# Kernel optimization log

Hardware: AMD Instinct MI355X
Metric: run time of the kernel (lower is better)

The kernel has to match this reference:

```python
import jax, jax.numpy as jnp
import numpy as np

N = 50000      # nodes
E = 500000     # edges
H = 128        # hidden_channels
P = 1024       # number of (src,dst) link pairs: z==1 and z==2 counts
L = 3          # num_layers
MAXZ = 1000


def setup_inputs() -> dict:
    key = jax.random.key(0)
    ks = jax.random.split(key, 16)
    # z: P src nodes (label 1), P dst nodes (label 2), rest random labels >= 3
    z = jnp.concatenate([
        jnp.ones((P,), jnp.int32),
        jnp.full((P,), 2, jnp.int32),
        jax.random.randint(ks[0], (N - 2 * P,), 3, MAXZ, dtype=jnp.int32),
    ])
    edge_index = jax.random.randint(ks[1], (2, E), 0, N, dtype=jnp.int32)
    batch = jnp.zeros((N,), jnp.int32)  # unused in executed branch
    s = 1.0 / np.sqrt(H)
    z_table = jax.random.normal(ks[2], (MAXZ, H), jnp.float32) * 0.1
    conv_Wl = jax.random.normal(ks[3], (L, H, H), jnp.float32) * s
    conv_bl = jax.random.normal(ks[4], (L, H), jnp.float32) * 0.01
    conv_Wr = jax.random.normal(ks[5], (L, H, H), jnp.float32) * s
    W0 = jax.random.normal(ks[6], (H, H), jnp.float32) * s
    b0 = jax.random.normal(ks[7], (H,), jnp.float32) * 0.01
    W1 = jax.random.normal(ks[8], (H, H), jnp.float32) * s
    b1 = jax.random.normal(ks[9], (H,), jnp.float32) * 0.01
    W2 = jax.random.normal(ks[10], (1, H), jnp.float32) * s
    b2 = jax.random.normal(ks[11], (1,), jnp.float32) * 0.01
    return dict(z=z, edge_index=edge_index, batch=batch, z_table=z_table,
                conv_Wl=conv_Wl, conv_bl=conv_bl, conv_Wr=conv_Wr,
                W0=W0, b0=b0, W1=W1, b1=b1, W2=W2, b2=b2)


def _sage_conv(x, Wl, bl, Wr, src, dst):
    # x: [2, N, H]; mean-aggregate neighbor messages then linear (PyG SAGEConv)
    msgs = x[:, src, :]  # [2, E, H] gather
    agg = jax.vmap(lambda m: jax.ops.segment_sum(m, dst, num_segments=N))(msgs)
    deg = jax.ops.segment_sum(jnp.ones((dst.shape[0],), x.dtype), dst, num_segments=N)
    agg = agg / jnp.maximum(deg, 1.0)[None, :, None]
    return agg @ Wl.T + bl + x @ Wr.T  # lin_l(mean) + bias + lin_r(x)


def reference(z, edge_index, batch, z_table, conv_Wl, conv_bl, conv_Wr,
              W0, b0, W1, b1, W2, b2):
    src, dst = edge_index[0], edge_index[1]
    # ([[1],[2]] == z).long() -> [2, N] in {0,1}; embed -> [2, N, H]
    lbl = (jnp.arange(1, 3, dtype=z.dtype)[:, None] == z[None, :]).astype(jnp.int32)
    x = z_table[lbl]
    for i in range(L - 1):
        x = jax.nn.relu(_sage_conv(x, conv_Wl[i], conv_bl[i], conv_Wr[i], src, dst))
    x = _sage_conv(x, conv_Wl[L - 1], conv_bl[L - 1], conv_Wr[L - 1], src, dst)
    h = jax.nn.relu(x @ W0.T + b0).sum(axis=0)  # [N, H]
    src_idx = jnp.nonzero(z == 1, size=P)[0]
    dst_idx = jnp.nonzero(z == 2, size=P)[0]
    p = h[src_idx] * h[dst_idx]                 # [P, H]
    return jax.nn.relu(p @ W1.T + b1) @ W2.T + b2  # [P, 1]
```

## Files before the change

kernel.cpp:

```cpp
#include <hip/hip_runtime.h>
#include <stdint.h>

#define HH 128
typedef unsigned long long ull;
typedef unsigned short u16;

__device__ __forceinline__ ull shfl_up64(ull v, int d) {
  unsigned lo = (unsigned)__shfl_up((int)(unsigned)(v & 0xffffffffULL), d);
  unsigned hi = (unsigned)__shfl_up((int)(unsigned)(v >> 32), d);
  return ((ull)hi << 32) | (ull)lo;
}
__device__ __forceinline__ ull shfl_down64(ull v, int d) {
  unsigned lo = (unsigned)__shfl_down((int)(unsigned)(v & 0xffffffffULL), d);
  unsigned hi = (unsigned)__shfl_down((int)(unsigned)(v >> 32), d);
  return ((ull)hi << 32) | (ull)lo;
}

__global__ __launch_bounds__(256) void k_ytab(
    const float* __restrict__ zt, const float* __restrict__ Wl0,
    const float* __restrict__ Wr0, const float* __restrict__ Wl2,
    const float* __restrict__ Wr2, const float* __restrict__ bl0,
    const float* __restrict__ bl1, float* __restrict__ y_l,
    float* __restrict__ y_rb, float* __restrict__ vecs_g,
    const int* __restrict__ z, int N, ull* __restrict__ cnt64,
    int* __restrict__ mark, int* __restrict__ status, int* __restrict__ bctr) {
  __shared__ float ztS[2][HH];
  __shared__ float vS[4][HH];
  __shared__ float xS[16][HH];
  __shared__ float wAS[32][HH + 1], wBS[32][HH + 1];
  int t = threadIdx.x;
  {
    int gid = blockIdx.x * 256 + t;
    int nthr = gridDim.x * 256;
    for (int n = gid; n < N; n += nthr) {
      cnt64[n] = 0ULL;
      mark[n] = (z[n] <= 2) ? 1 : 0;
    }
    if (gid < 64) status[gid] = 0;
    if (gid == 0) *bctr = 0;
  }
  ztS[t >> 7][t & 127] = zt[t];
  __syncthreads();
  int j = t & 127, half = t >> 7;
  int jw = t >> 3, kk0 = (t & 7) * 4;
  float accA = 0.f, accR = 0.f;
  for (int kt = 0; kt < 4; kt++) {
    __syncthreads();
#pragma unroll
    for (int q = 0; q < 4; q++) {
      int jj = q * 32 + jw;
      float4 va = *(const float4*)(Wl0 + (size_t)jj * HH + kt * 32 + kk0);
      float4 vb = *(const float4*)(Wr0 + (size_t)jj * HH + kt * 32 + kk0);
      wAS[kk0 + 0][jj] = va.x; wAS[kk0 + 1][jj] = va.y;
      wAS[kk0 + 2][jj] = va.z; wAS[kk0 + 3][jj] = va.w;
      wBS[kk0 + 0][jj] = vb.x; wBS[kk0 + 1][jj] = vb.y;
      wBS[kk0 + 2][jj] = vb.z; wBS[kk0 + 3][jj] = vb.w;
    }
    __syncthreads();
#pragma unroll
    for (int kk = 0; kk < 32; kk++) {
      float zk = ztS[half][kt * 32 + kk];
      accA = fmaf(zk, wAS[kk][j], accA);
      accR = fmaf(zk, wBS[kk][j], accR);
    }
  }
  __syncthreads();
  vS[half][j] = accA;
  vS[2 + half][j] = accR;
  __syncthreads();
  if (blockIdx.x == 0) {
    vecs_g[t] = vS[t >> 7][t & 127];
    vecs_g[256 + t] = vS[2 + (t >> 7)][t & 127];
  }
  int v0 = blockIdx.x * 16;
#pragma unroll
  for (int rep = 0; rep < 8; rep++) {
    int idx = t + rep * 256;
    int r = idx >> 7, jx = idx & 127;
    int v = v0 + r;
    int d = v >> 4, cnt = (v >> 1) & 7, sel = v & 1;
    float invd = 1.0f / (float)max(d, 1);
    float u1 = (float)cnt * invd, u0 = (float)(d - cnt) * invd;
    xS[r][jx] = fmaxf(fmaf(u0, vS[0][jx], fmaf(u1, vS[1][jx], bl0[jx] + vS[2 + sel][jx])), 0.f);
  }
  int rh = t >> 7;
  float al[8], ar[8];
#pragma unroll
  for (int q = 0; q < 8; q++) { al[q] = 0.f; ar[q] = 0.f; }
  for (int kt = 0; kt < 4; kt++) {
    __syncthreads();
#pragma unroll
    for (int q = 0; q < 4; q++) {
      int jj = q * 32 + jw;
      float4 va = *(const float4*)(Wl2 + (size_t)jj * HH + kt * 32 + kk0);
      float4 vb = *(const float4*)(Wr2 + (size_t)jj * HH + kt * 32 + kk0);
      wAS[kk0 + 0][jj] = va.x; wAS[kk0 + 1][jj] = va.y;
      wAS[kk0 + 2][jj] = va.z; wAS[kk0 + 3][jj] = va.w;
      wBS[kk0 + 0][jj] = vb.x; wBS[kk0 + 1][jj] = vb.y;
      wBS[kk0 + 2][jj] = vb.z; wBS[kk0 + 3][jj] = vb.w;
    }
    __syncthreads();
#pragma unroll
    for (int kk = 0; kk < 32; kk++) {
      float wl = wAS[kk][j], wr = wBS[kk][j];
#pragma unroll
      for (int q = 0; q < 8; q++) {
        float x = xS[rh * 8 + q][kt * 32 + kk];
        al[q] = fmaf(x, wl, al[q]);
        ar[q] = fmaf(x, wr, ar[q]);
      }
    }
  }
  float bb = bl1[j];
#pragma unroll
  for (int q = 0; q < 8; q++) {
    int v = v0 + rh * 8 + q;
    y_l[((size_t)v << 7) + j] = al[q];
    y_rb[((size_t)v << 7) + j] = ar[q] + bb;
  }
}

__global__ void k_edge(const int* __restrict__ z, const int* __restrict__ src,
                       const int* __restrict__ dst, int E,
                       ull* __restrict__ cnt64, int* __restrict__ mark,
                       int* __restrict__ pos) {
  int e = blockIdx.x * blockDim.x + threadIdx.x;
  if (e >= E) return;
  int s = src[e], d = dst[e];
  int zs = z[s];
  ull val = 1ULL | ((ull)(zs == 1) << 20) | ((ull)(zs == 2) << 40);
  ull old = atomicAdd(&cnt64[d], val);
  pos[e] = (int)(old & 0xFFFFF);
  if (z[d] <= 2) mark[s] = 1;
}

__global__ __launch_bounds__(256) void k_scanpost(
    const ull* __restrict__ cnt64, const int* __restrict__ mark,
    const int* __restrict__ z, int N, int P,
    int* __restrict__ rowptr, int* __restrict__ mlist, int* __restrict__ minv,
    int* __restrict__ plist, int* __restrict__ Rm, int4* __restrict__ pack,
    u16* __restrict__ keyN, int* __restrict__ bctr,
    ull* __restrict__ aggbuf, int* __restrict__ status) {
  __shared__ ull wsum[4];
  __shared__ int chunk_s;
  __shared__ ull excl_s;
  int t = threadIdx.x;
  if (t == 0) chunk_s = atomicAdd(bctr, 1);
  __syncthreads();
  int b = chunk_s;
  int base = b * 1024 + t * 4;
  ull l[4]; ull s = 0;
#pragma unroll
  for (int i = 0; i < 4; i++) {
    int idx = base + i; ull v = 0;
    if (idx < N) {
      int zz = z[idx];
      v = (cnt64[idx] & 0xFFFFFULL) | ((ull)mark[idx] << 20)
        | ((ull)(zz == 1) << 40) | ((ull)(zz == 2) << 52);
    }
    l[i] = s; s += v;
  }
  int lane = t & 63, wid = t >> 6;
  ull vi = s;
  for (int d2 = 1; d2 < 64; d2 <<= 1) { ull o = shfl_up64(vi, d2); if (lane >= d2) vi += o; }
  if (lane == 63) wsum[wid] = vi;
  __syncthreads();
  ull woff = 0;
  for (int w = 0; w < wid; w++) woff += wsum[w];
  ull thrbase = woff + vi - s;
  if (t == 0) {
    ull btot = wsum[0] + wsum[1] + wsum[2] + wsum[3];
    __hip_atomic_store(&aggbuf[b], btot, __ATOMIC_RELAXED, __HIP_MEMORY_SCOPE_AGENT);
    __hip_atomic_store(&status[b], 1, __ATOMIC_RELEASE, __HIP_MEMORY_SCOPE_AGENT);
  }
  if (t < 64) {
    ull excl = 0;
    for (int p = lane; p < b; p += 64) {
      while (__hip_atomic_load(&status[p], __ATOMIC_ACQUIRE, __HIP_MEMORY_SCOPE_AGENT) == 0)
        __builtin_amdgcn_s_sleep(1);
      excl += __hip_atomic_load(&aggbuf[p], __ATOMIC_RELAXED, __HIP_MEMORY_SCOPE_AGENT);
    }
    for (int o = 32; o > 0; o >>= 1) excl += shfl_down64(excl, o);
    if (lane == 0) excl_s = excl;
  }
  __syncthreads();
  ull blockbase = excl_s;
#pragma unroll
  for (int i = 0; i < 4; i++) {
    int idx = base + i;
    if (idx >= N) break;
    ull sf = blockbase + thrbase + l[i];
    int rp = (int)(sf & 0xFFFFF);
    int mp = (int)((sf >> 20) & 0xFFFFF);
    int r1 = (int)((sf >> 40) & 0xFFF);
    int r2 = (int)(sf >> 52);
    rowptr[idx] = rp;
    int mk = mark[idx];
    if (mk) { mlist[mp] = idx; minv[idx] = mp; }
    int zz = z[idx];
    if (zz == 1) plist[r1] = idx;
    else if (zz == 2) plist[P + r2] = idx;
    ull cv = cnt64[idx];
    int dd = (int)(cv & 0xFFFFF), c1 = (int)((cv >> 20) & 0xFFFFF), c2 = (int)((cv >> 40) & 0xFFFFF);
    pack[idx] = make_int4(dd, c1, c2, zz);
    int wcls = (zz == 1) ? 1 : ((zz == 2) ? 2 : 0);
    u16 key;
    if (dd < 64 && c1 < 8 && c2 < 8) key = (u16)(dd | (c1 << 6) | (c2 << 9) | (wcls << 12));
    else key = 0x8000;
    keyN[idx] = key;
    if (idx == N - 1) *Rm = mp + mk;
  }
}

__global__ void k_csrk(const int* __restrict__ src, const int* __restrict__ dst, int E,
                       const int* __restrict__ rowptr, const int* __restrict__ pos,
                       const u16* __restrict__ keyN, const int* __restrict__ mark,
                       ull* __restrict__ csrk) {
  int e = blockIdx.x * blockDim.x + threadIdx.x;
  if (e >= E) return;
  int d = dst[e];
  if (!mark[d]) return;
  int s = src[e];
  csrk[rowptr[d] + pos[e]] = (ull)(unsigned)s | ((ull)keyN[s] << 32);
}

__device__ __noinline__ float4 yrow_fb(const float* __restrict__ vecs,
    const float* __restrict__ bl0, const float* __restrict__ Wm,
    int j4, int d, int cnt, int sel) {
  float invd = 1.0f / (float)max(d, 1);
  float u1 = (float)cnt * invd, u0 = (float)(d - cnt) * invd;
  const float* Rv = vecs + (2 + sel) * HH;
  float4 acc = make_float4(0, 0, 0, 0);
  for (int k = 0; k < HH; k++) {
    float x = fmaxf(fmaf(u0, vecs[k], fmaf(u1, vecs[HH + k], bl0[k] + Rv[k])), 0.f);
    acc.x = fmaf(x, Wm[(j4 + 0) * HH + k], acc.x);
    acc.y = fmaf(x, Wm[(j4 + 1) * HH + k], acc.y);
    acc.z = fmaf(x, Wm[(j4 + 2) * HH + k], acc.z);
    acc.w = fmaf(x, Wm[(j4 + 3) * HH + k], acc.w);
  }
  return acc;
}

__device__ __forceinline__ float4 yl_fetch(ull cv, int ch, int chsel, int j4,
    const float* __restrict__ y_l, const int4* __restrict__ pack,
    const float* __restrict__ vecs, const float* __restrict__ bl0,
    const float* __restrict__ Wl2) {
  int key = (int)(cv >> 32);
  if (key & 0x8000) {
    int s = (int)(cv & 0xFFFFFFFFULL);
    int4 p = pack[s];
    int cc = ch ? p.z : p.y;
    int sel = (p.w == chsel) ? 1 : 0;
    return yrow_fb(vecs, bl0, Wl2, j4, p.x, cc, sel);
  }
  int cc = (key >> (6 + 3 * ch)) & 7;
  int sel = (((key >> 12) & 3) == chsel) ? 1 : 0;
  int row = ((key & 63) << 4) + (cc << 1) + sel;
  return *(const float4*)(y_l + ((size_t)row << 7) + j4);
}

__global__ __launch_bounds__(256) void k_agg2Y(const int4* __restrict__ pack,
    const ull* __restrict__ csrk, const float* __restrict__ y_l,
    const float* __restrict__ y_rb, const float* __restrict__ vecs,
    const float* __restrict__ bl0, const float* __restrict__ bl1,
    const float* __restrict__ Wl2, const float* __restrict__ Wr2,
    const int* __restrict__ rowptr, const int* __restrict__ mlist,
    const int* __restrict__ Rdev, float* __restrict__ x2c) {
  int gt = blockIdx.x * blockDim.x + threadIdx.x;
  int w = gt >> 6, lane = gt & 63;
  int nw = (gridDim.x * blockDim.x) >> 6;
  int T = *Rdev;
  int ch = lane >> 5, j4 = (lane & 31) * 4;
  int chsel = ch + 1;
  for (int task = w; task < T; task += nw) {
    int n = mlist[task];
    int4 pn = pack[n];
    int beg = rowptr[n], d = pn.x;
    float4 acc = make_float4(0, 0, 0, 0);
    int i = 0;
    for (; i + 4 <= d; i += 4) {
      ull c0 = csrk[beg + i], c1 = csrk[beg + i + 1];
      ull c2 = csrk[beg + i + 2], c3 = csrk[beg + i + 3];
      float4 v0 = yl_fetch(c0, ch, chsel, j4, y_l, pack, vecs, bl0, Wl2);
      float4 v1 = yl_fetch(c1, ch, chsel, j4, y_l, pack, vecs, bl0, Wl2);
      float4 v2 = yl_fetch(c2, ch, chsel, j4, y_l, pack, vecs, bl0, Wl2);
      float4 v3 = yl_fetch(c3, ch, chsel, j4, y_l, pack, vecs, bl0, Wl2);
      acc.x += v0.x + v1.x + v2.x + v3.x;
      acc.y += v0.y + v1.y + v2.y + v3.y;
      acc.z += v0.z + v1.z + v2.z + v3.z;
      acc.w += v0.w + v1.w + v2.w + v3.w;
    }
    for (; i < d; i++) {
      float4 v0 = yl_fetch(csrk[beg + i], ch, chsel, j4, y_l, pack, vecs, bl0, Wl2);
      acc.x += v0.x; acc.y += v0.y; acc.z += v0.z; acc.w += v0.w;
    }
    float inv = 1.0f / (float)max(d, 1);
    int ccn = ch ? pn.z : pn.y;
    int seln = (pn.w == chsel) ? 1 : 0;
    float4 yr;
    if (pn.x < 64 && ccn < 8) {
      yr = *(const float4*)(y_rb + ((size_t)(((pn.x << 3) + ccn) * 2 + seln) << 7) + j4);
    } else {
      yr = yrow_fb(vecs, bl0, Wr2, j4, pn.x, ccn, seln);
      yr.x += bl1[j4]; yr.y += bl1[j4 + 1]; yr.z += bl1[j4 + 2]; yr.w += bl1[j4 + 3];
    }
    float4 o;
    o.x = fmaxf(fmaf(acc.x, inv, yr.x), 0.f);
    o.y = fmaxf(fmaf(acc.y, inv, yr.y), 0.f);
    o.z = fmaxf(fmaf(acc.z, inv, yr.z), 0.f);
    o.w = fmaxf(fmaf(acc.w, inv, yr.w), 0.f);
    *(float4*)(x2c + (size_t)task * 256 + ch * HH + j4) = o;
  }
}

__global__ __launch_bounds__(256) void k_agg3(const float* __restrict__ x2c,
    const ull* __restrict__ csrk, const int* __restrict__ rowptr,
    const int4* __restrict__ pack, const int* __restrict__ plist,
    const int* __restrict__ minv, int T, float* __restrict__ aggp) {
  int gt = blockIdx.x * blockDim.x + threadIdx.x;
  int w = gt >> 6, lane = gt & 63;
  int nw = (gridDim.x * blockDim.x) >> 6;
  int j4 = lane * 4;
  for (int task = w; task < T; task += nw) {
    int n = plist[task];
    int beg = rowptr[n], d = pack[n].x;
    float4 acc = make_float4(0, 0, 0, 0);
    int i = 0;
    for (; i + 4 <= d; i += 4) {
      int m0 = minv[(int)(csrk[beg + i] & 0xFFFFFFFFULL)];
      int m1 = minv[(int)(csrk[beg + i + 1] & 0xFFFFFFFFULL)];
      int m2 = minv[(int)(csrk[beg + i + 2] & 0xFFFFFFFFULL)];
      int m3 = minv[(int)(csrk[beg + i + 3] & 0xFFFFFFFFULL)];
      float4 v0 = *(const float4*)(x2c + (size_t)m0 * 256 + j4);
      float4 v1 = *(const float4*)(x2c + (size_t)m1 * 256 + j4);
      float4 v2 = *(const float4*)(x2c + (size_t)m2 * 256 + j4);
      float4 v3 = *(const float4*)(x2c + (size_t)m3 * 256 + j4);
      acc.x += v0.x + v1.x + v2.x + v3.x;
      acc.y += v0.y + v1.y + v2.y + v3.y;
      acc.z += v0.z + v1.z + v2.z + v3.z;
      acc.w += v0.w + v1.w + v2.w + v3.w;
    }
    for (; i < d; i++) {
      int m0 = minv[(int)(csrk[beg + i] & 0xFFFFFFFFULL)];
      float4 v0 = *(const float4*)(x2c + (size_t)m0 * 256 + j4);
      acc.x += v0.x; acc.y += v0.y; acc.z += v0.z; acc.w += v0.w;
    }
    float inv = 1.0f / (float)max(d, 1);
    float4 o = make_float4(acc.x * inv, acc.y * inv, acc.z * inv, acc.w * inv);
    *(float4*)(aggp + (size_t)task * 256 + j4) = o;
  }
}

#define G3 4
__global__ __launch_bounds__(256) void k_gemm3FP(const float* __restrict__ aggp,
    const float* __restrict__ x2c, const float* __restrict__ Wl3,
    const float* __restrict__ Wr3, const float* __restrict__ W0,
    const float* __restrict__ W1, const float* __restrict__ bl2,
    const float* __restrict__ b0, const float* __restrict__ b1,
    const float* __restrict__ W2, const float* __restrict__ b2,
    const int* __restrict__ plist, const int* __restrict__ minv,
    int P, float* __restrict__ out) {
  __shared__ float aS[G3][256], xS[G3][256], x3S[G3][256];
  __shared__ float wAS[32][HH + 1], wBS[32][HH + 1];
  __shared__ float pS[2][HH];
  __shared__ float wred[4];
  int t = threadIdx.x;
  int i0 = blockIdx.x * 2;
  int tsk[G3] = { i0, i0 + 1, P + i0, P + i0 + 1 };
  int j = t & 127, c = t >> 7;
#pragma unroll
  for (int g = 0; g < G3; g++) {
    int i = tsk[g];
    aS[g][t] = aggp[(size_t)i * 256 + t];
    xS[g][t] = x2c[(size_t)minv[plist[i]] * 256 + t];
  }
  float acc[G3];
#pragma unroll
  for (int g = 0; g < G3; g++) acc[g] = bl2[j];
  int jw = t >> 3;
  int kk0 = (t & 7) * 4;
  for (int kt = 0; kt < 4; kt++) {
    __syncthreads();
#pragma unroll
    for (int q = 0; q < 4; q++) {
      int jj = q * 32 + jw;
      float4 va = *(const float4*)(Wl3 + (size_t)jj * HH + kt * 32 + kk0);
      float4 vb = *(const float4*)(Wr3 + (size_t)jj * HH + kt * 32 + kk0);
      wAS[kk0 + 0][jj] = va.x; wAS[kk0 + 1][jj] = va.y;
      wAS[kk0 + 2][jj] = va.z; wAS[kk0 + 3][jj] = va.w;
      wBS[kk0 + 0][jj] = vb.x; wBS[kk0 + 1][jj] = vb.y;
      wBS[kk0 + 2][jj] = vb.z; wBS[kk0 + 3][jj] = vb.w;
    }
    __syncthreads();
#pragma unroll
    for (int kk = 0; kk < 32; kk++) {
      int k = kt * 32 + kk;
      float wl = wAS[kk][j], wr = wBS[kk][j];
#pragma unroll
      for (int g = 0; g < G3; g++)
        acc[g] = fmaf(aS[g][c * HH + k], wl, fmaf(xS[g][c * HH + k], wr, acc[g]));
    }
  }
#pragma unroll
  for (int g = 0; g < G3; g++) x3S[g][t] = acc[g];
  float acc2[G3];
#pragma unroll
  for (int g = 0; g < G3; g++) acc2[g] = b0[j];
  for (int kt = 0; kt < 4; kt++) {
    __syncthreads();
#pragma unroll
    for (int q = 0; q < 4; q++) {
      int jj = q * 32 + jw;
      float4 v0 = *(const float4*)(W0 + (size_t)jj * HH + kt * 32 + kk0);
      wAS[kk0 + 0][jj] = v0.x; wAS[kk0 + 1][jj] = v0.y;
      wAS[kk0 + 2][jj] = v0.z; wAS[kk0 + 3][jj] = v0.w;
    }
    __syncthreads();
#pragma unroll
    for (int kk = 0; kk < 32; kk++) {
      int k = kt * 32 + kk;
      float w0v = wAS[kk][j];
#pragma unroll
      for (int g = 0; g < G3; g++)
        acc2[g] = fmaf(x3S[g][c * HH + k], w0v, acc2[g]);
    }
  }
  __syncthreads();
#pragma unroll
  for (int g = 0; g < G3; g++) x3S[g][t] = fmaxf(acc2[g], 0.f);
  __syncthreads();
  {
    int p = t >> 7, jx = t & 127;
    float hs = x3S[p][jx] + x3S[p][HH + jx];
    float hd = x3S[2 + p][jx] + x3S[2 + p][HH + jx];
    pS[p][jx] = hs * hd;
  }
  float acc3 = b1[j];
  for (int kt = 0; kt < 4; kt++) {
    __syncthreads();
#pragma unroll
    for (int q = 0; q < 4; q++) {
      int jj = q * 32 + jw;
      float4 v = *(const float4*)(W1 + (size_t)jj * HH + kt * 32 + kk0);
      wAS[kk0 + 0][jj] = v.x; wAS[kk0 + 1][jj] = v.y;
      wAS[kk0 + 2][jj] = v.z; wAS[kk0 + 3][jj] = v.w;
    }
    __syncthreads();
#pragma unroll
    for (int kk = 0; kk < 32; kk++)
      acc3 = fmaf(pS[c][kt * 32 + kk], wAS[kk][j], acc3);
  }
  float v = fmaxf(acc3, 0.f) * W2[j];
  for (int off = 32; off > 0; off >>= 1) v += __shfl_down(v, off);
  int wid = t >> 6, lane = t & 63;
  if (lane == 0) wred[wid] = v;
  __syncthreads();
  if (t == 0) out[i0] = wred[0] + wred[1] + b2[0];
  else if (t == 128) out[i0 + 1] = wred[2] + wred[3] + b2[0];
}

extern "C" void kernel_launch(void* const* d_in, const int* in_sizes, int n_in,
                              void* d_out, int out_size, void* d_ws, size_t ws_size,
                              hipStream_t stream) {
  const int* z = (const int*)d_in[0];
  const int* ei = (const int*)d_in[1];
  const float* z_table = (const float*)d_in[3];
  const float* conv_Wl = (const float*)d_in[4];
  const float* conv_bl = (const float*)d_in[5];
  const float* conv_Wr = (const float*)d_in[6];
  const float* W0 = (const float*)d_in[7];
  const float* b0 = (const float*)d_in[8];
  const float* W1 = (const float*)d_in[9];
  const float* b1 = (const float*)d_in[10];
  const float* W2 = (const float*)d_in[11];
  const float* b2 = (const float*)d_in[12];
  float* out = (float*)d_out;

  int N = in_sizes[0];
  int E = in_sizes[1] / 2;
  int P = out_size;
  int P2 = 2 * P;
  const int* srcA = ei;
  const int* dstA = ei + E;

  char* basep = (char*)d_ws;
  size_t off = 0;
  auto alloc = [&](size_t bytes) -> char* {
    off = (off + 255) & ~(size_t)255;
    char* pp = basep + off; off += bytes; return pp;
  };
  float* y_l   = (float*)alloc((size_t)1024 * HH * 4);
  float* y_rb  = (float*)alloc((size_t)1024 * HH * 4);
  float* vecs  = (float*)alloc((size_t)4 * HH * 4);
  float* x2c   = (float*)alloc((size_t)N * 256 * 4);
  float* aggp  = (float*)alloc((size_t)P2 * 256 * 4);
  ull*   cnt64 = (ull*)alloc((size_t)N * 8);
  int*   mark  = (int*)alloc((size_t)N * 4);
  int*   pos   = (int*)alloc((size_t)E * 4);
  int*   rowptr= (int*)alloc((size_t)N * 4);
  int*   mlist = (int*)alloc((size_t)N * 4);
  int*   minv  = (int*)alloc((size_t)N * 4);
  int*   plist = (int*)alloc((size_t)P2 * 4);
  ull*   csrk  = (ull*)alloc((size_t)E * 8);
  ull*   aggbuf= (ull*)alloc(64 * 8);
  int*   status= (int*)alloc(64 * 4);
  int*   bctr  = (int*)alloc(256);
  int*   Rm_dev= (int*)alloc(256);
  u16*   keyN  = (u16*)alloc((size_t)N * 2);
  int4*  pack  = (int4*)alloc((size_t)N * 16);
  (void)ws_size; (void)n_in;

  k_ytab<<<64, 256, 0, stream>>>(z_table, conv_Wl, conv_Wr,
                                 conv_Wl + HH * HH, conv_Wr + HH * HH,
                                 conv_bl, conv_bl + HH, y_l, y_rb, vecs,
                                 z, N, cnt64, mark, status, bctr);
  k_edge<<<(E + 255) / 256, 256, 0, stream>>>(z, srcA, dstA, E, cnt64, mark, pos);
  int nb = (N + 1023) / 1024;
  k_scanpost<<<nb, 256, 0, stream>>>(cnt64, mark, z, N, P, rowptr, mlist, minv,
                                     plist, Rm_dev, pack, keyN, bctr, aggbuf, status);
  k_csrk<<<(E + 255) / 256, 256, 0, stream>>>(srcA, dstA, E, rowptr, pos, keyN, mark, csrk);
  k_agg2Y<<<2048, 256, 0, stream>>>(pack, csrk, y_l, y_rb, vecs, conv_bl, conv_bl + HH,
                                    conv_Wl + HH * HH, conv_Wr + HH * HH,
                                    rowptr, mlist, Rm_dev, x2c);
  k_agg3<<<512, 256, 0, stream>>>(x2c, csrk, rowptr, pack, plist, minv, P2, aggp);
  k_gemm3FP<<<P / 2, 256, 0, stream>>>(aggp, x2c, conv_Wl + 2 * HH * HH,
                                       conv_Wr + 2 * HH * HH, W0, W1,
                                       conv_bl + 2 * HH, b0, b1, W2, b2,
                                       plist, minv, P, out);
}
```

Baseline: 130.6 us.

## Fold W0 into last SAGE layer weights and precompute fused bias

Because the last SAGE layer has no activation before the W0 linear, the weights are precomposed (W0·Wl3, W0·Wr3) and the bias (W0·bl2 + b0) inside the setup kernel, which already runs early. The tail kernel then does one fused GEMM instead of two chained ones and handles one pair per block with P blocks instead of two pairs per block. This trades extra weight-precompute work in k_ytab and a reduction in per-block weight reuse for less tail compute.

```diff
diff --git a/kernel.cpp b/kernel.cpp
--- a/kernel.cpp
+++ b/kernel.cpp
@@ -20,8 +20,12 @@
     const float* __restrict__ zt, const float* __restrict__ Wl0,
     const float* __restrict__ Wr0, const float* __restrict__ Wl2,
     const float* __restrict__ Wr2, const float* __restrict__ bl0,
-    const float* __restrict__ bl1, float* __restrict__ y_l,
-    float* __restrict__ y_rb, float* __restrict__ vecs_g,
+    const float* __restrict__ bl1, const float* __restrict__ Wl3,
+    const float* __restrict__ Wr3, const float* __restrict__ W0,
+    const float* __restrict__ bl2, const float* __restrict__ b0,
+    float* __restrict__ y_l, float* __restrict__ y_rb,
+    float* __restrict__ vecs_g, float* __restrict__ Wcl,
+    float* __restrict__ Wcr, float* __restrict__ b03,
     const int* __restrict__ z, int N, ull* __restrict__ cnt64,
     int* __restrict__ mark, int* __restrict__ status, int* __restrict__ bctr) {
   __shared__ float ztS[2][HH];
@@ -117,6 +121,46 @@
     int v = v0 + rh * 8 + q;
     y_l[((size_t)v << 7) + j] = al[q];
     y_rb[((size_t)v << 7) + j] = ar[q] + bb;
+  }
+  if (blockIdx.x < 32) {
+    __syncthreads();
+    const float* Wsrc = (blockIdx.x < 16) ? Wl3 : Wr3;
+    float* Wdst = (blockIdx.x < 16) ? Wcl : Wcr;
+    int j0 = (blockIdx.x & 15) * 8;
+    {
+      float4 w0v = *(const float4*)(W0 + (size_t)j0 * HH + t * 4);
+      int r = (t * 4) >> 7, m = (t * 4) & 127;
+      xS[r][m] = w0v.x; xS[r][m + 1] = w0v.y; xS[r][m + 2] = w0v.z; xS[r][m + 3] = w0v.w;
+    }
+    __syncthreads();
+    int k = t & 127, h = t >> 7;
+    float acc[4] = {0.f, 0.f, 0.f, 0.f};
+    for (int m = 0; m < HH; m++) {
+      float v = Wsrc[(size_t)m * HH + k];
+#pragma unroll
+      for (int r = 0; r < 4; r++) acc[r] = fmaf(xS[h * 4 + r][m], v, acc[r]);
+    }
+#pragma unroll
+    for (int r = 0; r < 4; r++) Wdst[(size_t)(j0 + h * 4 + r) * HH + k] = acc[r];
+  } else if (blockIdx.x == 32) {
+    __syncthreads();
+    if (t < HH) vS[0][t] = bl2[t];
+    float acc = 0.f;
+    for (int kt = 0; kt < 4; kt++) {
+      __syncthreads();
+#pragma unroll
+      for (int q = 0; q < 4; q++) {
+        int jj = q * 32 + jw;
+        float4 v0 = *(const float4*)(W0 + (size_t)jj * HH + kt * 32 + kk0);
+        wAS[kk0 + 0][jj] = v0.x; wAS[kk0 + 1][jj] = v0.y;
+        wAS[kk0 + 2][jj] = v0.z; wAS[kk0 + 3][jj] = v0.w;
+      }
+      __syncthreads();
+#pragma unroll
+      for (int kk = 0; kk < 32; kk++)
+        acc = fmaf(vS[0][kt * 32 + kk], wAS[kk][j], acc);
+    }
+    if (t < HH) b03[j] = acc + b0[j];
   }
 }
 
@@ -351,41 +395,37 @@
   }
 }
 
-#define G3 4
-__global__ __launch_bounds__(256) void k_gemm3FP(const float* __restrict__ aggp,
-    const float* __restrict__ x2c, const float* __restrict__ Wl3,
-    const float* __restrict__ Wr3, const float* __restrict__ W0,
-    const float* __restrict__ W1, const float* __restrict__ bl2,
-    const float* __restrict__ b0, const float* __restrict__ b1,
+__global__ __launch_bounds__(256) void k_tail(const float* __restrict__ aggp,
+    const float* __restrict__ x2c, const float* __restrict__ Wcl,
+    const float* __restrict__ Wcr, const float* __restrict__ b03,
+    const float* __restrict__ W1, const float* __restrict__ b1,
     const float* __restrict__ W2, const float* __restrict__ b2,
     const int* __restrict__ plist, const int* __restrict__ minv,
     int P, float* __restrict__ out) {
-  __shared__ float aS[G3][256], xS[G3][256], x3S[G3][256];
   __shared__ float wAS[32][HH + 1], wBS[32][HH + 1];
-  __shared__ float pS[2][HH];
-  __shared__ float wred[4];
+  __shared__ float aS[2][256], xS[2][256], hS[2][256];
+  __shared__ float pS[HH];
+  __shared__ float wred[2];
   int t = threadIdx.x;
-  int i0 = blockIdx.x * 2;
-  int tsk[G3] = { i0, i0 + 1, P + i0, P + i0 + 1 };
+  int i0 = blockIdx.x;
+  int tsk[2] = { i0, P + i0 };
   int j = t & 127, c = t >> 7;
 #pragma unroll
-  for (int g = 0; g < G3; g++) {
+  for (int g = 0; g < 2; g++) {
     int i = tsk[g];
     aS[g][t] = aggp[(size_t)i * 256 + t];
     xS[g][t] = x2c[(size_t)minv[plist[i]] * 256 + t];
   }
-  float acc[G3];
-#pragma unroll
-  for (int g = 0; g < G3; g++) acc[g] = bl2[j];
-  int jw = t >> 3;
-  int kk0 = (t & 7) * 4;
+  float bias = b03[j];
+  float acc0 = bias, acc1 = bias;
+  int jw = t >> 3, kk0 = (t & 7) * 4;
   for (int kt = 0; kt < 4; kt++) {
     __syncthreads();
 #pragma unroll
     for (int q = 0; q < 4; q++) {
       int jj = q * 32 + jw;
-      float4 va = *(const float4*)(Wl3 + (size_t)jj * HH + kt * 32 + kk0);
-      float4 vb = *(const float4*)(Wr3 + (size_t)jj * HH + kt * 32 + kk0);
+      float4 va = *(const float4*)(Wcl + (size_t)jj * HH + kt * 32 + kk0);
+      float4 vb = *(const float4*)(Wcr + (size_t)jj * HH + kt * 32 + kk0);
       wAS[kk0 + 0][jj] = va.x; wAS[kk0 + 1][jj] = va.y;
       wAS[kk0 + 2][jj] = va.z; wAS[kk0 + 3][jj] = va.w;
       wBS[kk0 + 0][jj] = vb.x; wBS[kk0 + 1][jj] = vb.y;
@@ -396,45 +436,15 @@
     for (int kk = 0; kk < 32; kk++) {
       int k = kt * 32 + kk;
       float wl = wAS[kk][j], wr = wBS[kk][j];
-#pragma unroll
-      for (int g = 0; g < G3; g++)
-        acc[g] = fmaf(aS[g][c * HH + k], wl, fmaf(xS[g][c * HH + k], wr, acc[g]));
-    }
-  }
-#pragma unroll
-  for (int g = 0; g < G3; g++) x3S[g][t] = acc[g];
-  float acc2[G3];
-#pragma unroll
-  for (int g = 0; g < G3; g++) acc2[g] = b0[j];
-  for (int kt = 0; kt < 4; kt++) {
-    __syncthreads();
-#pragma unroll
-    for (int q = 0; q < 4; q++) {
-      int jj = q * 32 + jw;
-      float4 v0 = *(const float4*)(W0 + (size_t)jj * HH + kt * 32 + kk0);
-      wAS[kk0 + 0][jj] = v0.x; wAS[kk0 + 1][jj] = v0.y;
-      wAS[kk0 + 2][jj] = v0.z; wAS[kk0 + 3][jj] = v0.w;
-    }
-    __syncthreads();
-#pragma unroll
-    for (int kk = 0; kk < 32; kk++) {
-      int k = kt * 32 + kk;
-      float w0v = wAS[kk][j];
-#pragma unroll
-      for (int g = 0; g < G3; g++)
-        acc2[g] = fmaf(x3S[g][c * HH + k], w0v, acc2[g]);
-    }
-  }
-  __syncthreads();
-#pragma unroll
-  for (int g = 0; g < G3; g++) x3S[g][t] = fmaxf(acc2[g], 0.f);
-  __syncthreads();
-  {
-    int p = t >> 7, jx = t & 127;
-    float hs = x3S[p][jx] + x3S[p][HH + jx];
-    float hd = x3S[2 + p][jx] + x3S[2 + p][HH + jx];
-    pS[p][jx] = hs * hd;
-  }
+      acc0 = fmaf(aS[0][c * HH + k], wl, fmaf(xS[0][c * HH + k], wr, acc0));
+      acc1 = fmaf(aS[1][c * HH + k], wl, fmaf(xS[1][c * HH + k], wr, acc1));
+    }
+  }
+  hS[0][t] = fmaxf(acc0, 0.f);
+  hS[1][t] = fmaxf(acc1, 0.f);
+  __syncthreads();
+  if (t < HH)
+    pS[t] = (hS[0][t] + hS[0][HH + t]) * (hS[1][t] + hS[1][HH + t]);
   float acc3 = b1[j];
   for (int kt = 0; kt < 4; kt++) {
     __syncthreads();
@@ -448,15 +458,14 @@
     __syncthreads();
 #pragma unroll
     for (int kk = 0; kk < 32; kk++)
-      acc3 = fmaf(pS[c][kt * 32 + kk], wAS[kk][j], acc3);
+      acc3 = fmaf(pS[kt * 32 + kk], wAS[kk][j], acc3);
   }
   float v = fmaxf(acc3, 0.f) * W2[j];
+  int lane = t & 63, wid = t >> 6;
   for (int off = 32; off > 0; off >>= 1) v += __shfl_down(v, off);
-  int wid = t >> 6, lane = t & 63;
-  if (lane == 0) wred[wid] = v;
+  if (wid < 2 && lane == 0) wred[wid] = v;
   __syncthreads();
   if (t == 0) out[i0] = wred[0] + wred[1] + b2[0];
-  else if (t == 128) out[i0 + 1] = wred[2] + wred[3] + b2[0];
 }
 
 extern "C" void kernel_launch(void* const* d_in, const int* in_sizes, int n_in,
@@ -492,6 +501,9 @@
   float* y_l   = (float*)alloc((size_t)1024 * HH * 4);
   float* y_rb  = (float*)alloc((size_t)1024 * HH * 4);
   float* vecs  = (float*)alloc((size_t)4 * HH * 4);
+  float* Wcl   = (float*)alloc((size_t)HH * HH * 4);
+  float* Wcr   = (float*)alloc((size_t)HH * HH * 4);
+  float* b03   = (float*)alloc((size_t)HH * 4);
   float* x2c   = (float*)alloc((size_t)N * 256 * 4);
   float* aggp  = (float*)alloc((size_t)P2 * 256 * 4);
   ull*   cnt64 = (ull*)alloc((size_t)N * 8);
@@ -512,7 +524,10 @@
 
   k_ytab<<<64, 256, 0, stream>>>(z_table, conv_Wl, conv_Wr,
                                  conv_Wl + HH * HH, conv_Wr + HH * HH,
-                                 conv_bl, conv_bl + HH, y_l, y_rb, vecs,
+                                 conv_bl, conv_bl + HH,
+                                 conv_Wl + 2 * HH * HH, conv_Wr + 2 * HH * HH,
+                                 W0, conv_bl + 2 * HH, b0,
+                                 y_l, y_rb, vecs, Wcl, Wcr, b03,
                                  z, N, cnt64, mark, status, bctr);
   k_edge<<<(E + 255) / 256, 256, 0, stream>>>(z, srcA, dstA, E, cnt64, mark, pos);
   int nb = (N + 1023) / 1024;
@@ -523,8 +538,6 @@
                                     conv_Wl + HH * HH, conv_Wr + HH * HH,
                                     rowptr, mlist, Rm_dev, x2c);
   k_agg3<<<512, 256, 0, stream>>>(x2c, csrk, rowptr, pack, plist, minv, P2, aggp);
-  k_gemm3FP<<<P / 2, 256, 0, stream>>>(aggp, x2c, conv_Wl + 2 * HH * HH,
-                                       conv_Wr + 2 * HH * HH, W0, W1,
-                                       conv_bl + 2 * HH, b0, b1, W2, b2,
-                                       plist, minv, P, out);
-}
+  k_tail<<<P, 256, 0, stream>>>(aggp, x2c, Wcl, Wcr, b03, W1, b1, W2, b2,
+                                plist, minv, P, out);
+}
```

After: 129.3 us. Within noise of the previous version (-1.0%).
